# Kernel tuning notes

Measured on AMD Instinct MI355X. Metric: run time of the kernel, lower is better.

## Reference

```python
import jax, jax.numpy as jnp
import numpy as np

DIM = 256
HEADS = 8
PS = 8  # patch/window size
EPS = 1e-5


def _ln(x, g, b):
    m = x.mean(-1, keepdims=True)
    v = x.var(-1, keepdims=True)
    return (x - m) / jnp.sqrt(v + EPS) * g + b


def setup_inputs() -> dict:
    key = jax.random.key(0)
    ks = jax.random.split(key, 10)
    B, C, H, W = 4, DIM, 256, 256
    s = 0.02
    return {
        "y_lf": jax.random.normal(ks[0], (B, C, H, W), jnp.float32),
        "y_hf": jax.random.normal(ks[1], (B, C, H, W), jnp.float32),
        "g_lf": jnp.ones((C,), jnp.float32),
        "b_lf": jnp.zeros((C,), jnp.float32),
        "g_hf": jnp.ones((C,), jnp.float32),
        "b_hf": jnp.zeros((C,), jnp.float32),
        "Wq": jax.random.normal(ks[2], (C, C), jnp.float32) * s,
        "bq": jnp.zeros((C,), jnp.float32),
        "Wk": jax.random.normal(ks[3], (C, C), jnp.float32) * s,
        "bk": jnp.zeros((C,), jnp.float32),
        "Wv": jax.random.normal(ks[4], (C, C), jnp.float32) * s,
        "bv": jnp.zeros((C,), jnp.float32),
        "Wo": jax.random.normal(ks[5], (C, C), jnp.float32) * s,
        "bo": jnp.zeros((C,), jnp.float32),
    }


def reference(y_lf, y_hf, g_lf, b_lf, g_hf, b_hf, Wq, bq, Wk, bk, Wv, bv, Wo, bo):
    B, C, H, W = y_lf.shape
    ps = PS
    hd = C // HEADS
    nH, nW = H // ps, W // ps

    def win_tokens(x):
        # (B,C,H,W) -> (B*nH*nW, ps*ps, C)
        x = x.reshape(B, C, nH, ps, nW, ps)
        return x.transpose(0, 2, 4, 3, 5, 1).reshape(-1, ps * ps, C)

    lf = win_tokens(y_lf)
    hf = win_tokens(y_hf)  # residual + V source (un-normalized, as in torch code)

    q = _ln(lf, g_lf, b_lf) @ Wq.T + bq
    k = _ln(hf, g_hf, b_hf) @ Wk.T + bk
    v = hf @ Wv.T + bv

    BW, L, _ = q.shape
    q = q.reshape(BW, L, HEADS, hd)
    k = k.reshape(BW, L, HEADS, hd)
    v = v.reshape(BW, L, HEADS, hd)

    scale = 1.0 / np.sqrt(hd).astype(np.float32)
    scores = jnp.einsum('bqhd,bkhd->bhqk', q, k) * scale
    attn = jax.nn.softmax(scores, axis=-1)
    o = jnp.einsum('bhqk,bkhd->bqhd', attn, v).reshape(BW, L, C)
    o = o @ Wo.T + bo + hf  # out_proj + residual

    # window_reverse: (B*nH*nW, ps*ps, C) -> (B,C,H,W)
    o = o.reshape(B, nH, nW, ps, ps, C)
    o = o.transpose(0, 5, 1, 3, 2, 4).reshape(B, C, H, W)
    return o
```

## Files before the change

### kernel.cpp

```cpp
#include <hip/hip_runtime.h>

typedef float  f4     __attribute__((ext_vector_type(4)));
typedef float  f32x4  __attribute__((ext_vector_type(4)));
typedef short  short8 __attribute__((ext_vector_type(8)));
typedef __bf16 bf16x8 __attribute__((ext_vector_type(8)));
typedef int    int4v  __attribute__((ext_vector_type(4)));
typedef unsigned short us4 __attribute__((ext_vector_type(4)));

__device__ __forceinline__ unsigned short f2bf(float f) {
    unsigned int u = __builtin_bit_cast(unsigned int, f);
    u += 0x7FFFu + ((u >> 16) & 1u);
    return (unsigned short)(u >> 16);
}
__device__ __forceinline__ float bf2f(unsigned short h) {
    unsigned int u = ((unsigned int)h) << 16;
    return __builtin_bit_cast(float, u);
}
__device__ __forceinline__ f32x4 mfma_bf16(short8 a, short8 b, f32x4 c) {
    return __builtin_amdgcn_mfma_f32_16x16x32_bf16(
        __builtin_bit_cast(bf16x8, a), __builtin_bit_cast(bf16x8, b), c, 0, 0, 0);
}
__device__ __forceinline__ int cvt_pk_bf16(float lo, float hi) {
    int d;
    asm volatile("v_cvt_pk_bf16_f32 %0, %1, %2" : "=v"(d) : "v"(lo), "v"(hi));
    return d;
}
__device__ __forceinline__ int bperm(int addr, int src) {
    return __builtin_amdgcn_ds_bpermute(addr, src);
}

__global__ void pcaf_precvt(const float* __restrict__ Wq, const float* __restrict__ bq,
                            const float* __restrict__ Wk, const float* __restrict__ bk,
                            const float* __restrict__ Wv, const float* __restrict__ Wo,
                            const float* __restrict__ g_lf, const float* __restrict__ b_lf,
                            const float* __restrict__ g_hf, const float* __restrict__ b_hf,
                            void* __restrict__ ws) {
    const int mat  = blockIdx.x >> 8;
    const int row  = blockIdx.x & 255;
    const int lane = threadIdx.x;
    const float* W = (mat == 0) ? Wq : (mat == 1) ? Wk : (mat == 2) ? Wv : Wo;
    f4 w = *(const f4*)(W + row * 256 + lane * 4);
    f4 wp = w;
    if (mat < 2) {
        const float* g = mat ? g_hf : g_lf;
        f4 gg = *(const f4*)(g + lane * 4);
        wp = w * gg;
    }
    us4 u;
    u[0] = f2bf(wp[0]); u[1] = f2bf(wp[1]); u[2] = f2bf(wp[2]); u[3] = f2bf(wp[3]);
    {
        const int ct   = row >> 4;
        const int l15r = row & 15;
        const int k_   = lane >> 3;
        const int g_   = (lane >> 1) & 3;
        const int e4   = (lane & 1) * 4;
        unsigned short* dst = (unsigned short*)ws + mat * 65536 +
                              (((ct * 8 + k_) * 64) + g_ * 16 + l15r) * 8 + e4;
        *(us4*)dst = u;
    }
    if (mat < 2) {
        const float* b = mat ? b_hf : b_lf;
        f4 bb = *(const f4*)(b + lane * 4);
        float rsum = wp[0] + wp[1] + wp[2] + wp[3];
        float cb   = bb[0] * w[0] + bb[1] * w[1] + bb[2] * w[2] + bb[3] * w[3];
        #pragma unroll
        for (int d = 1; d < 64; d <<= 1) {
            rsum += __shfl_xor(rsum, d);
            cb   += __shfl_xor(cb, d);
        }
        if (lane == 0) {
            float* cons = (float*)((char*)ws + 524288);
            cons[mat * 512 + row]       = rsum;
            cons[mat * 512 + 256 + row] = cb + (mat ? bk[row] : bq[row]);
        }
    }
}

constexpr int RS  = 528;
constexpr int HWC = 65536;
constexpr int Wd  = 256;
constexpr int OA  = 0;
constexpr int OB  = 67584;
constexpr int OS  = 135168;

struct AccW { f32x4 a[4][2]; };

__device__ __forceinline__ AccW gemmW(const char* base,
                                      const unsigned short* __restrict__ Wbw,
                                      int lane, int g, int l15) {
    AccW r;
    f32x4 z = {0.f, 0.f, 0.f, 0.f};
    #pragma unroll
    for (int m = 0; m < 4; ++m) { r.a[m][0] = z; r.a[m][1] = z; }
    #pragma unroll
    for (int half = 0; half < 2; ++half) {
        short8 w0[4], w1[4];
        #pragma unroll
        for (int k = 0; k < 4; ++k) {
            w0[k] = *(const short8*)(Wbw + (half * 4 + k) * 512 + lane * 8);
            w1[k] = *(const short8*)(Wbw + 4096 + (half * 4 + k) * 512 + lane * 8);
        }
        #pragma unroll
        for (int k = 0; k < 4; ++k) {
            #pragma unroll
            for (int m = 0; m < 4; ++m) {
                short8 am = *(const short8*)(base + (16 * m + l15) * RS +
                                             ((half * 4 + k) * 32 + g * 8) * 2);
                r.a[m][0] = mfma_bf16(am, w0[k], r.a[m][0]);
                r.a[m][1] = mfma_bf16(am, w1[k], r.a[m][1]);
            }
        }
    }
    return r;
}

__global__ __attribute__((amdgpu_flat_work_group_size(1024, 1024)))
void pcaf8_kernel(
    const float* __restrict__ y_lf, const float* __restrict__ y_hf,
    const float* __restrict__ bv, const float* __restrict__ bo,
    const void* __restrict__ ws, float* __restrict__ out)
{
    __shared__ __align__(16) char sm[137216];

    const unsigned short* wsq = (const unsigned short*)ws;
    const unsigned short* wsk = wsq + 65536;
    const unsigned short* wsv = wsq + 131072;
    const unsigned short* wso = wsq + 196608;
    const float* cons = (const float*)((const char*)ws + 524288);

    const int tid = threadIdx.x;
    const int bid = blockIdx.x;
    const int wi  = ((bid & 7) << 8) | (bid >> 3);
    const int bb  = wi >> 9;
    const int nh  = (wi >> 4) & 31;
    const int nwp = wi & 15;
    const long pair_base = (long)bb * 256 * HWC + (long)(nh * 8) * Wd + nwp * 16;

    const int wave = tid >> 6;
    const int win  = wave >> 3;
    const int head = wave & 7;
    const int lane = tid & 63;
    const int g    = lane >> 4;
    const int l15  = lane & 15;
    const int c0   = 32 * head + l15;
    const int ro   = win * 64;

    {
        f4 lv[8], hv[8];
        #pragma unroll
        for (int it = 0; it < 4; ++it) {
            int q2  = it * 1024 + tid;
            int c2  = q2 >> 5;
            int ph  = (q2 >> 2) & 7;
            int pw4 = (q2 & 3) * 4;
            long go = pair_base + (long)(2 * c2) * HWC + ph * Wd + pw4;
            lv[2 * it]     = *(const f4*)(y_lf + go);
            lv[2 * it + 1] = *(const f4*)(y_lf + go + HWC);
            hv[2 * it]     = *(const f4*)(y_hf + go);
            hv[2 * it + 1] = *(const f4*)(y_hf + go + HWC);
        }
        #pragma unroll
        for (int it = 0; it < 4; ++it) {
            int q2  = it * 1024 + tid;
            int c2  = q2 >> 5;
            int ph  = (q2 >> 2) & 7;
            int pw4 = (q2 & 3) * 4;
            int tok0 = (pw4 >> 3) * 64 + ph * 8 + (pw4 & 7);
            #pragma unroll
            for (int j = 0; j < 4; ++j) {
                unsigned int lvv = (unsigned int)f2bf(lv[2 * it][j]) | ((unsigned int)f2bf(lv[2 * it + 1][j]) << 16);
                unsigned int hvv = (unsigned int)f2bf(hv[2 * it][j]) | ((unsigned int)f2bf(hv[2 * it + 1][j]) << 16);
                *(unsigned int*)(sm + OA + (tok0 + j) * RS + c2 * 4) = lvv;
                *(unsigned int*)(sm + OB + (tok0 + j) * RS + c2 * 4) = hvv;
            }
        }
    }
    __syncthreads();

    {
        const int t = tid >> 3, j = tid & 7;
        #pragma unroll
        for (int pass = 0; pass < 2; ++pass) {
            const int base = pass ? OB : OA;
            float sum = 0.f, ss = 0.f;
            #pragma unroll
            for (int r = 0; r < 4; ++r) {
                short8 raw = *(const short8*)(sm + base + t * RS + (j * 32 + r * 8) * 2);
                #pragma unroll
                for (int e = 0; e < 8; ++e) { float f = bf2f((unsigned short)raw[e]); sum += f; ss += f * f; }
            }
            sum += __shfl_xor(sum, 1); ss += __shfl_xor(ss, 1);
            sum += __shfl_xor(sum, 2); ss += __shfl_xor(ss, 2);
            sum += __shfl_xor(sum, 4); ss += __shfl_xor(ss, 4);
            float mean = sum * (1.f / 256.f);
            float rstd = rsqrtf(ss * (1.f / 256.f) - mean * mean + 1e-5f);
            if (j == 0) {
                float* S = (float*)(sm + OS);
                S[pass * 256 + t]       = mean;
                S[pass * 256 + 128 + t] = rstd;
            }
        }
    }

    AccW qacc = gemmW(sm + OA + ro * RS, wsq + head * 8192, lane, g, l15);

    unsigned int resp[4][2][2];
    #pragma unroll
    for (int m = 0; m < 4; ++m)
        #pragma unroll
        for (int n = 0; n < 2; ++n)
            #pragma unroll
            for (int jh = 0; jh < 2; ++jh) {
                unsigned int lo = *(const unsigned short*)(sm + OB + (ro + 16 * m + 4 * g + 2 * jh) * RS + (c0 + 16 * n) * 2);
                unsigned int hi = *(const unsigned short*)(sm + OB + (ro + 16 * m + 4 * g + 2 * jh + 1) * RS + (c0 + 16 * n) * 2);
                resp[m][n][jh] = lo | (hi << 16);
            }

    int vp[4][2][2];
    {
        AccW vacc = gemmW(sm + OB + ro * RS, wsv + head * 8192, lane, g, l15);
        float bv0 = bv[c0], bv1 = bv[c0 + 16];
        #pragma unroll
        for (int m = 0; m < 4; ++m) {
            vp[m][0][0] = cvt_pk_bf16(vacc.a[m][0][0] + bv0, vacc.a[m][0][1] + bv0);
            vp[m][0][1] = cvt_pk_bf16(vacc.a[m][0][2] + bv0, vacc.a[m][0][3] + bv0);
            vp[m][1][0] = cvt_pk_bf16(vacc.a[m][1][0] + bv1, vacc.a[m][1][1] + bv1);
            vp[m][1][1] = cvt_pk_bf16(vacc.a[m][1][2] + bv1, vacc.a[m][1][3] + bv1);
        }
    }
    __syncthreads();

    {
        const float* S = (const float*)(sm + OS);
        const float SCALE = 0.17677669529663687f;
        float rs0 = cons[c0], rs1 = cons[c0 + 16];
        float cb0 = cons[256 + c0], cb1 = cons[256 + c0 + 16];
        #pragma unroll
        for (int m = 0; m < 4; ++m)
            #pragma unroll
            for (int i = 0; i < 4; ++i) {
                int t = ro + 16 * m + 4 * g + i;
                float mean = S[t], rstd = S[128 + t];
                float v0 = (rstd * (qacc.a[m][0][i] - mean * rs0) + cb0) * SCALE;
                float v1 = (rstd * (qacc.a[m][1][i] - mean * rs1) + cb1) * SCALE;
                *(unsigned short*)(sm + OA + t * RS + c0 * 2)        = f2bf(v0);
                *(unsigned short*)(sm + OA + t * RS + (c0 + 16) * 2) = f2bf(v1);
            }
    }

    AccW kacc = gemmW(sm + OB + ro * RS, wsk + head * 8192, lane, g, l15);
    __syncthreads();

    {
        const float* S = (const float*)(sm + OS);
        float rs0 = cons[512 + c0], rs1 = cons[512 + c0 + 16];
        float cb0 = cons[768 + c0], cb1 = cons[768 + c0 + 16];
        #pragma unroll
        for (int m = 0; m < 4; ++m)
            #pragma unroll
            for (int i = 0; i < 4; ++i) {
                int t = ro + 16 * m + 4 * g + i;
                float mean = S[256 + t], rstd = S[384 + t];
                float v0 = rstd * (kacc.a[m][0][i] - mean * rs0) + cb0;
                float v1 = rstd * (kacc.a[m][1][i] - mean * rs1) + cb1;
                *(unsigned short*)(sm + OB + t * RS + c0 * 2)        = f2bf(v0);
                *(unsigned short*)(sm + OB + t * RS + (c0 + 16) * 2) = f2bf(v1);
            }
    }
    __syncthreads();

    {
        short8 kf[4], qf[4];
        #pragma unroll
        for (int x = 0; x < 4; ++x) {
            kf[x] = *(const short8*)(sm + OB + (ro + 16 * x + l15) * RS + (32 * head + 8 * g) * 2);
            qf[x] = *(const short8*)(sm + OA + (ro + 16 * x + l15) * RS + (32 * head + 8 * g) * 2);
        }
        __syncthreads();

        f32x4 z = {0.f, 0.f, 0.f, 0.f};
        const int a0 = ((2 * (g & 1)) * 16 + l15) * 4;
        const int a1 = a0 + 64;
        const bool ghi = (g >> 1) & 1;

        short8 vf[2][2];
        #pragma unroll
        for (int kk = 0; kk < 2; ++kk)
            #pragma unroll
            for (int n2 = 0; n2 < 2; ++n2) {
                int4v t;
                #pragma unroll
                for (int j = 0; j < 4; ++j) {
                    int ad = (j >> 1) ? a1 : a0;
                    int v0 = bperm(ad, vp[2 * kk][n2][j & 1]);
                    int v1 = bperm(ad, vp[2 * kk + 1][n2][j & 1]);
                    t[j] = ghi ? v1 : v0;
                }
                vf[kk][n2] = __builtin_bit_cast(short8, t);
            }

        f32x4 o[4][2];
        #pragma unroll
        for (int c = 0; c < 4; ++c) { o[c][0] = z; o[c][1] = z; }

        #pragma unroll
        for (int c = 0; c < 4; ++c) {
            f32x4 stc[4];
            #pragma unroll
            for (int nk = 0; nk < 4; ++nk)
                stc[nk] = mfma_bf16(kf[nk], qf[c], z);

            float mx = stc[0][0];
            #pragma unroll
            for (int nk = 0; nk < 4; ++nk)
                #pragma unroll
                for (int i = 0; i < 4; ++i) mx = fmaxf(mx, stc[nk][i]);
            mx = fmaxf(mx, __shfl_xor(mx, 16));
            mx = fmaxf(mx, __shfl_xor(mx, 32));
            float sum = 0.f;
            #pragma unroll
            for (int nk = 0; nk < 4; ++nk)
                #pragma unroll
                for (int i = 0; i < 4; ++i) {
                    float e = __expf(stc[nk][i] - mx);
                    stc[nk][i] = e;
                    sum += e;
                }
            sum += __shfl_xor(sum, 16);
            sum += __shfl_xor(sum, 32);
            float is = 1.f / sum;

            int pq[4][2];
            #pragma unroll
            for (int nk = 0; nk < 4; ++nk) {
                pq[nk][0] = cvt_pk_bf16(stc[nk][0] * is, stc[nk][1] * is);
                pq[nk][1] = cvt_pk_bf16(stc[nk][2] * is, stc[nk][3] * is);
            }

            #pragma unroll
            for (int kk = 0; kk < 2; ++kk) {
                int4v t;
                #pragma unroll
                for (int j = 0; j < 4; ++j) {
                    int ad = (j >> 1) ? a1 : a0;
                    int v0 = bperm(ad, pq[2 * kk][j & 1]);
                    int v1 = bperm(ad, pq[2 * kk + 1][j & 1]);
                    t[j] = ghi ? v1 : v0;
                }
                short8 pf = __builtin_bit_cast(short8, t);
                o[c][0] = mfma_bf16(pf, vf[kk][0], o[c][0]);
                o[c][1] = mfma_bf16(pf, vf[kk][1], o[c][1]);
            }
        }

        #pragma unroll
        for (int c = 0; c < 4; ++c)
            #pragma unroll
            for (int i = 0; i < 4; ++i) {
                int t = ro + 16 * c + 4 * g + i;
                *(unsigned short*)(sm + OA + t * RS + c0 * 2)        = f2bf(o[c][0][i]);
                *(unsigned short*)(sm + OA + t * RS + (c0 + 16) * 2) = f2bf(o[c][1][i]);
            }
    }
    __syncthreads();

    AccW oacc = gemmW(sm + OA + ro * RS, wso + head * 8192, lane, g, l15);
    __syncthreads();

    {
        float bo0 = bo[c0], bo1 = bo[c0 + 16];
        #pragma unroll
        for (int n = 0; n < 2; ++n) {
            float bon = n ? bo1 : bo0;
            int cout = c0 + 16 * n;
            #pragma unroll
            for (int m = 0; m < 4; ++m) {
                int ph  = 2 * m + (g >> 1);
                int pw4 = 4 * (g & 1);
                f4 ov;
                #pragma unroll
                for (int i = 0; i < 4; ++i) {
                    float rv = bf2f((unsigned short)((resp[m][n][i >> 1] >> (16 * (i & 1))) & 0xFFFF));
                    ov[i] = oacc.a[m][n][i] + bon + rv;
                }
                *(f4*)(sm + (cout * 132 + ph * 16 + win * 8 + pw4) * 4) = ov;
            }
        }
    }
    __syncthreads();

    {
        #pragma unroll
        for (int it = 0; it < 8; ++it) {
            int idx = it * 1024 + tid;
            int c   = idx >> 5;
            int rem = idx & 31;
            int ph  = rem >> 2;
            int l4  = rem & 3;
            f4 v = *(const f4*)(sm + (c * 132 + ph * 16 + l4 * 4) * 4);
            *(f4*)(out + pair_base + (long)c * HWC + ph * Wd + l4 * 4) = v;
        }
    }
}

extern "C" void kernel_launch(void* const* d_in, const int* in_sizes, int n_in,
                              void* d_out, int out_size, void* d_ws, size_t ws_size,
                              hipStream_t stream) {
    (void)in_sizes; (void)n_in; (void)out_size; (void)ws_size;
    const float* y_lf = (const float*)d_in[0];
    const float* y_hf = (const float*)d_in[1];
    const float* g_lf = (const float*)d_in[2];
    const float* b_lf = (const float*)d_in[3];
    const float* g_hf = (const float*)d_in[4];
    const float* b_hf = (const float*)d_in[5];
    const float* Wq   = (const float*)d_in[6];
    const float* bq   = (const float*)d_in[7];
    const float* Wk   = (const float*)d_in[8];
    const float* bk   = (const float*)d_in[9];
    const float* Wv   = (const float*)d_in[10];
    const float* bv   = (const float*)d_in[11];
    const float* Wo   = (const float*)d_in[12];
    const float* bo   = (const float*)d_in[13];
    float* out = (float*)d_out;

    pcaf_precvt<<<dim3(1024), dim3(64), 0, stream>>>(
        Wq, bq, Wk, bk, Wv, Wo, g_lf, b_lf, g_hf, b_hf, d_ws);
    pcaf8_kernel<<<dim3(2048), dim3(1024), 0, stream>>>(
        y_lf, y_hf, bv, bo, d_ws, out);
}
```

Measured before the change: 508.3 us.

## Swizzle LDS token tiles, batch Q/K GEMMs, and store output directly

Applies an XOR swizzle on the column byte offset, keyed by row, to every shared-memory access of the token tiles, aiming to reduce LDS bank conflicts in the MFMA operand loads. Computes the K and Q projections back to back before a single barrier, which removes one __syncthreads. Drops the shared-memory staging of the output and writes 16-byte vectors straight to global memory, removing two barriers but producing narrower, less coalesced stores. Also pins waves_per_eu to 4, which caps register use and may cause spills.

```diff
diff --git a/kernel.cpp b/kernel.cpp
--- a/kernel.cpp
+++ b/kernel.cpp
@@ -27,6 +27,9 @@
 }
 __device__ __forceinline__ int bperm(int addr, int src) {
     return __builtin_amdgcn_ds_bpermute(addr, src);
+}
+__device__ __forceinline__ int swz(int row, int B) {
+    return B ^ (((row >> 3) & 7) << 4);
 }
 
 __global__ void pcaf_precvt(const float* __restrict__ Wq, const float* __restrict__ bq,
@@ -104,8 +107,9 @@
         for (int k = 0; k < 4; ++k) {
             #pragma unroll
             for (int m = 0; m < 4; ++m) {
-                short8 am = *(const short8*)(base + (16 * m + l15) * RS +
-                                             ((half * 4 + k) * 32 + g * 8) * 2);
+                int row = 16 * m + l15;
+                short8 am = *(const short8*)(base + row * RS +
+                                             swz(row, ((half * 4 + k) * 32 + g * 8) * 2));
                 r.a[m][0] = mfma_bf16(am, w0[k], r.a[m][0]);
                 r.a[m][1] = mfma_bf16(am, w1[k], r.a[m][1]);
             }
@@ -114,8 +118,8 @@
     return r;
 }
 
-__global__ __attribute__((amdgpu_flat_work_group_size(1024, 1024)))
-void pcaf8_kernel(
+__global__ __attribute__((amdgpu_flat_work_group_size(1024, 1024), amdgpu_waves_per_eu(4, 4)))
+void pcaf9_kernel(
     const float* __restrict__ y_lf, const float* __restrict__ y_hf,
     const float* __restrict__ bv, const float* __restrict__ bo,
     const void* __restrict__ ws, float* __restrict__ out)
@@ -168,10 +172,12 @@
             int tok0 = (pw4 >> 3) * 64 + ph * 8 + (pw4 & 7);
             #pragma unroll
             for (int j = 0; j < 4; ++j) {
+                int row = tok0 + j;
                 unsigned int lvv = (unsigned int)f2bf(lv[2 * it][j]) | ((unsigned int)f2bf(lv[2 * it + 1][j]) << 16);
                 unsigned int hvv = (unsigned int)f2bf(hv[2 * it][j]) | ((unsigned int)f2bf(hv[2 * it + 1][j]) << 16);
-                *(unsigned int*)(sm + OA + (tok0 + j) * RS + c2 * 4) = lvv;
-                *(unsigned int*)(sm + OB + (tok0 + j) * RS + c2 * 4) = hvv;
+                int col = swz(row, c2 * 4);
+                *(unsigned int*)(sm + OA + row * RS + col) = lvv;
+                *(unsigned int*)(sm + OB + row * RS + col) = hvv;
             }
         }
     }
@@ -185,7 +191,7 @@
             float sum = 0.f, ss = 0.f;
             #pragma unroll
             for (int r = 0; r < 4; ++r) {
-                short8 raw = *(const short8*)(sm + base + t * RS + (j * 32 + r * 8) * 2);
+                short8 raw = *(const short8*)(sm + base + t * RS + swz(t, (j * 32 + r * 8) * 2));
                 #pragma unroll
                 for (int e = 0; e < 8; ++e) { float f = bf2f((unsigned short)raw[e]); sum += f; ss += f * f; }
             }
@@ -202,8 +208,6 @@
         }
     }
 
-    AccW qacc = gemmW(sm + OA + ro * RS, wsq + head * 8192, lane, g, l15);
-
     unsigned int resp[4][2][2];
     #pragma unroll
     for (int m = 0; m < 4; ++m)
@@ -211,8 +215,9 @@
         for (int n = 0; n < 2; ++n)
             #pragma unroll
             for (int jh = 0; jh < 2; ++jh) {
-                unsigned int lo = *(const unsigned short*)(sm + OB + (ro + 16 * m + 4 * g + 2 * jh) * RS + (c0 + 16 * n) * 2);
-                unsigned int hi = *(const unsigned short*)(sm + OB + (ro + 16 * m + 4 * g + 2 * jh + 1) * RS + (c0 + 16 * n) * 2);
+                int r0 = ro + 16 * m + 4 * g + 2 * jh;
+                unsigned int lo = *(const unsigned short*)(sm + OB + r0 * RS + swz(r0, (c0 + 16 * n) * 2));
+                unsigned int hi = *(const unsigned short*)(sm + OB + (r0 + 1) * RS + swz(r0 + 1, (c0 + 16 * n) * 2));
                 resp[m][n][jh] = lo | (hi << 16);
             }
 
@@ -228,6 +233,9 @@
             vp[m][1][1] = cvt_pk_bf16(vacc.a[m][1][2] + bv1, vacc.a[m][1][3] + bv1);
         }
     }
+
+    AccW kacc = gemmW(sm + OB + ro * RS, wsk + head * 8192, lane, g, l15);
+    AccW qacc = gemmW(sm + OA + ro * RS, wsq + head * 8192, lane, g, l15);
     __syncthreads();
 
     {
@@ -243,28 +251,21 @@
                 float mean = S[t], rstd = S[128 + t];
                 float v0 = (rstd * (qacc.a[m][0][i] - mean * rs0) + cb0) * SCALE;
                 float v1 = (rstd * (qacc.a[m][1][i] - mean * rs1) + cb1) * SCALE;
-                *(unsigned short*)(sm + OA + t * RS + c0 * 2)        = f2bf(v0);
-                *(unsigned short*)(sm + OA + t * RS + (c0 + 16) * 2) = f2bf(v1);
-            }
-    }
-
-    AccW kacc = gemmW(sm + OB + ro * RS, wsk + head * 8192, lane, g, l15);
-    __syncthreads();
-
-    {
-        const float* S = (const float*)(sm + OS);
-        float rs0 = cons[512 + c0], rs1 = cons[512 + c0 + 16];
-        float cb0 = cons[768 + c0], cb1 = cons[768 + c0 + 16];
+                *(unsigned short*)(sm + OA + t * RS + swz(t, c0 * 2))        = f2bf(v0);
+                *(unsigned short*)(sm + OA + t * RS + swz(t, (c0 + 16) * 2)) = f2bf(v1);
+            }
+        float rk0 = cons[512 + c0], rk1 = cons[512 + c0 + 16];
+        float ck0 = cons[768 + c0], ck1 = cons[768 + c0 + 16];
         #pragma unroll
         for (int m = 0; m < 4; ++m)
             #pragma unroll
             for (int i = 0; i < 4; ++i) {
                 int t = ro + 16 * m + 4 * g + i;
                 float mean = S[256 + t], rstd = S[384 + t];
-                float v0 = rstd * (kacc.a[m][0][i] - mean * rs0) + cb0;
-                float v1 = rstd * (kacc.a[m][1][i] - mean * rs1) + cb1;
-                *(unsigned short*)(sm + OB + t * RS + c0 * 2)        = f2bf(v0);
-                *(unsigned short*)(sm + OB + t * RS + (c0 + 16) * 2) = f2bf(v1);
+                float v0 = rstd * (kacc.a[m][0][i] - mean * rk0) + ck0;
+                float v1 = rstd * (kacc.a[m][1][i] - mean * rk1) + ck1;
+                *(unsigned short*)(sm + OB + t * RS + swz(t, c0 * 2))        = f2bf(v0);
+                *(unsigned short*)(sm + OB + t * RS + swz(t, (c0 + 16) * 2)) = f2bf(v1);
             }
     }
     __syncthreads();
@@ -273,8 +274,10 @@
         short8 kf[4], qf[4];
         #pragma unroll
         for (int x = 0; x < 4; ++x) {
-            kf[x] = *(const short8*)(sm + OB + (ro + 16 * x + l15) * RS + (32 * head + 8 * g) * 2);
-            qf[x] = *(const short8*)(sm + OA + (ro + 16 * x + l15) * RS + (32 * head + 8 * g) * 2);
+            int row = ro + 16 * x + l15;
+            int col = swz(row, (32 * head + 8 * g) * 2);
+            kf[x] = *(const short8*)(sm + OB + row * RS + col);
+            qf[x] = *(const short8*)(sm + OA + row * RS + col);
         }
         __syncthreads();
 
@@ -358,16 +361,15 @@
             #pragma unroll
             for (int i = 0; i < 4; ++i) {
                 int t = ro + 16 * c + 4 * g + i;
-                *(unsigned short*)(sm + OA + t * RS + c0 * 2)        = f2bf(o[c][0][i]);
-                *(unsigned short*)(sm + OA + t * RS + (c0 + 16) * 2) = f2bf(o[c][1][i]);
+                *(unsigned short*)(sm + OA + t * RS + swz(t, c0 * 2))        = f2bf(o[c][0][i]);
+                *(unsigned short*)(sm + OA + t * RS + swz(t, (c0 + 16) * 2)) = f2bf(o[c][1][i]);
             }
     }
     __syncthreads();
 
-    AccW oacc = gemmW(sm + OA + ro * RS, wso + head * 8192, lane, g, l15);
-    __syncthreads();
-
-    {
+    {
+        AccW oacc = gemmW(sm + OA + ro * RS, wso + head * 8192, lane, g, l15);
+        const long win_base = pair_base + win * 8;
         float bo0 = bo[c0], bo1 = bo[c0 + 16];
         #pragma unroll
         for (int n = 0; n < 2; ++n) {
@@ -375,30 +377,16 @@
             int cout = c0 + 16 * n;
             #pragma unroll
             for (int m = 0; m < 4; ++m) {
-                int ph  = 2 * m + (g >> 1);
-                int pw4 = 4 * (g & 1);
+                int tok0 = 16 * m + 4 * g;
+                int ph = tok0 >> 3, pw = tok0 & 7;
                 f4 ov;
                 #pragma unroll
                 for (int i = 0; i < 4; ++i) {
                     float rv = bf2f((unsigned short)((resp[m][n][i >> 1] >> (16 * (i & 1))) & 0xFFFF));
                     ov[i] = oacc.a[m][n][i] + bon + rv;
                 }
-                *(f4*)(sm + (cout * 132 + ph * 16 + win * 8 + pw4) * 4) = ov;
-            }
-        }
-    }
-    __syncthreads();
-
-    {
-        #pragma unroll
-        for (int it = 0; it < 8; ++it) {
-            int idx = it * 1024 + tid;
-            int c   = idx >> 5;
-            int rem = idx & 31;
-            int ph  = rem >> 2;
-            int l4  = rem & 3;
-            f4 v = *(const f4*)(sm + (c * 132 + ph * 16 + l4 * 4) * 4);
-            *(f4*)(out + pair_base + (long)c * HWC + ph * Wd + l4 * 4) = v;
+                *(f4*)(out + win_base + (long)cout * HWC + ph * Wd + pw) = ov;
+            }
         }
     }
 }
@@ -425,6 +413,6 @@
 
     pcaf_precvt<<<dim3(1024), dim3(64), 0, stream>>>(
         Wq, bq, Wk, bk, Wv, Wo, g_lf, b_lf, g_hf, b_hf, d_ws);
-    pcaf8_kernel<<<dim3(2048), dim3(1024), 0, stream>>>(
+    pcaf9_kernel<<<dim3(2048), dim3(1024), 0, stream>>>(
         y_lf, y_hf, bv, bo, d_ws, out);
 }
```

New measurement: 658.7 us. 29.6% more time.
